# Kernel optimization log

Hardware: AMD Instinct MI355X
Metric: run time of the kernel (lower is better)

The kernel has to match this reference:

```python
import jax, jax.numpy as jnp
import numpy as np

B, N, D, H, K = 8, 1024, 1024, 64, 20


def setup_inputs() -> dict:
    key = jax.random.key(0)
    ks = jax.random.split(key, 8)
    s = 0.05
    return {
        "f1": jax.random.normal(ks[0], (B, N, D), jnp.float32),
        "f2": jax.random.normal(ks[1], (B, N, D), jnp.float32),
        "W1a": jax.random.normal(ks[2], (D, H), jnp.float32) * s,
        "b1a": jnp.zeros((H,), jnp.float32),
        "W2a": jax.random.normal(ks[3], (H, H), jnp.float32) * s,
        "b2a": jnp.zeros((H,), jnp.float32),
        "W1b": jax.random.normal(ks[4], (H, H), jnp.float32) * s,
        "b1b": jnp.zeros((H,), jnp.float32),
        "W2b": jax.random.normal(ks[5], (H, H), jnp.float32) * s,
        "b2b": jnp.zeros((H,), jnp.float32),
        "k": K,
    }


def _knn_idx(f, k):
    # f: [N, D] -> indices [N, k] of k nearest neighbors (self excluded)
    sq = jnp.sum(f * f, axis=-1)                      # [N]
    d = sq[:, None] + sq[None, :] - 2.0 * (f @ f.T)   # [N, N] squared dists
    n = f.shape[0]
    d = d + jnp.eye(n, dtype=f.dtype) * jnp.float32(1e10)  # exclude self-loop
    _, idx = jax.lax.top_k(-d, k)                     # smallest distances
    return idx


def _gin_layer(x, idx, W1, b1, W2, b2):
    # GINConv with eps=0: MLP(x + sum_{j in N(i)} x_j)
    agg = jnp.sum(x[idx], axis=1)                     # [N, D] neighbor-sum
    h = x + agg
    h = jnp.maximum(h @ W1 + b1, 0.0) @ W2 + b2
    return h


def reference(f1, f2, W1a, b1a, W2a, b2a, W1b, b1b, W2b, b2b, k):
    def encode(f):
        idx = _knn_idx(f, k)
        h = _gin_layer(f, idx, W1a, b1a, W2a, b2a)
        h = _gin_layer(h, idx, W1b, b1b, W2b, b2b)
        return h

    def per_sample(a, b):
        z1 = encode(a)                                # [N, H]
        z2 = encode(b)                                # [N, H]
        sim = z1 @ z2.T                               # [N, N]
        return jax.nn.softmax(sim, axis=1)

    return jax.vmap(per_sample)(f1, f2)               # [B, N, N]
```

## Files before the change

### kernel.cpp

```cpp
#include <hip/hip_runtime.h>
#include <hip/hip_bf16.h>
#include <math.h>

#define BATCH 8
#define NPTS  1024
#define DIM   1024
#define HID   64
#define KNN   20
#define NMAT  16
#define KPACK 3072

typedef __attribute__((ext_vector_type(8))) short short8;
typedef __attribute__((ext_vector_type(4))) float floatx4;

__device__ __forceinline__ const float* mat_base(const float* f1, const float* f2, int m) {
    return (m < BATCH) ? (f1 + (size_t)m * NPTS * DIM)
                       : (f2 + (size_t)(m - BATCH) * NPTS * DIM);
}

__device__ __forceinline__ unsigned short f2bf_bits(float v) {
    __hip_bfloat16 h = __float2bfloat16(v);
    return *(unsigned short*)&h;
}
__device__ __forceinline__ float bfbits2f(unsigned short b) {
    union { unsigned u; float f; } c; c.u = ((unsigned)b) << 16; return c.f;
}

__global__ __launch_bounds__(256) void split_ymlp_kernel(const float* __restrict__ f1,
                                                         const float* __restrict__ f2,
                                                         const float* __restrict__ W,
                                                         unsigned short* __restrict__ H,
                                                         float* __restrict__ sq,
                                                         float* __restrict__ y) {
    int row0 = blockIdx.x * 64;
    int m = row0 >> 10;
    const float* A = mat_base(f1, f2, m) + (size_t)(row0 & (NPTS - 1)) * DIM;
    unsigned short* Hb = H + (size_t)row0 * KPACK;
    __shared__ float As[64][20];
    __shared__ float Ws[16][HID];
    int tid = threadIdx.x;
    int r = tid >> 2, cq = (tid & 3) * 4;
    int ty = tid >> 4, tx = tid & 15;
    float acc[4][4];
    #pragma unroll
    for (int i = 0; i < 4; ++i)
        #pragma unroll
        for (int j = 0; j < 4; ++j) acc[i][j] = 0.f;
    float sqp = 0.f;
    unsigned short* Hr = Hb + (size_t)r * KPACK + cq;

    for (int kk = 0; kk < DIM; kk += 16) {
        float4 a = *(const float4*)&A[(size_t)r * DIM + kk + cq];
        {
            float vv[4] = {a.x, a.y, a.z, a.w};
            unsigned short h1[4], h2[4], h3[4];
            #pragma unroll
            for (int c = 0; c < 4; ++c) {
                unsigned short b1 = f2bf_bits(vv[c]);
                float r1 = vv[c] - bfbits2f(b1);
                unsigned short b2 = f2bf_bits(r1);
                float r2 = r1 - bfbits2f(b2);
                unsigned short b3 = f2bf_bits(r2);
                h1[c] = b1; h2[c] = b2; h3[c] = b3;
            }
            *(ushort4*)&Hr[kk]        = *(ushort4*)&h1[0];
            *(ushort4*)&Hr[1024 + kk] = *(ushort4*)&h2[0];
            *(ushort4*)&Hr[2048 + kk] = *(ushort4*)&h3[0];
            sqp += a.x * a.x + a.y * a.y + a.z * a.z + a.w * a.w;
        }
        *(float4*)&As[r][cq] = a;
        {
            int d = tid >> 4, hh = (tid & 15) * 4;
            *(float4*)&Ws[d][hh] = *(const float4*)&W[(size_t)(kk + d) * HID + hh];
        }
        __syncthreads();
        #pragma unroll
        for (int k = 0; k < 16; ++k) {
            float av[4];
            #pragma unroll
            for (int ii = 0; ii < 4; ++ii) av[ii] = As[ty * 4 + ii][k];
            float4 w = *(const float4*)&Ws[k][tx * 4];
            #pragma unroll
            for (int ii = 0; ii < 4; ++ii) {
                acc[ii][0] += av[ii] * w.x;
                acc[ii][1] += av[ii] * w.y;
                acc[ii][2] += av[ii] * w.z;
                acc[ii][3] += av[ii] * w.w;
            }
        }
        __syncthreads();
    }
    sqp += __shfl_down(sqp, 1);
    sqp += __shfl_down(sqp, 2);
    if ((tid & 3) == 0) sq[row0 + r] = sqp;
    #pragma unroll
    for (int ii = 0; ii < 4; ++ii)
        *(float4*)&y[(size_t)(row0 + ty * 4 + ii) * HID + tx * 4] = *(float4*)&acc[ii][0];
}

__global__ __launch_bounds__(256) void gram_mfma_kernel(const unsigned short* __restrict__ H,
                                                        const float* __restrict__ sq,
                                                        float* __restrict__ dist) {
    int bid = blockIdx.x;
    int xcd = bid & 7;
    int g = bid >> 3;
    int m = xcd + 8 * (g & 1);
    int t = g >> 1;
    int bi = 0;
    { int a = t; while (a >= 8 - bi) { a -= 8 - bi; ++bi; } t = a; }
    int bj = bi + t;
    int ti = bi << 7, tj = bj << 7;

    const unsigned short* Hm = H + (size_t)m * NPTS * KPACK;

    __shared__ __align__(16) unsigned short Asl[24 * 512];
    __shared__ __align__(16) unsigned short Bsl[24 * 512];

    int tid = threadIdx.x;
    int w = tid >> 6, lane = tid & 63;
    int wi = w >> 1, wj = w & 1;
    int r16 = lane & 15, kc = lane >> 4;

    floatx4 acc[4][4];
    #pragma unroll
    for (int a = 0; a < 4; ++a)
        #pragma unroll
        for (int b = 0; b < 4; ++b) acc[a][b] = (floatx4)0.f;

    for (int kk = 0; kk < 1024; kk += 32) {
        __syncthreads();
        #pragma unroll
        for (int c = 0; c < 6; ++c) {
            int ca = w * 6 + c;
            int seg = ca >> 3;
            int rb  = ca & 7;
            size_t koff = (size_t)(seg << 10) + kk + kc * 8;
            const unsigned short* ga = Hm + (size_t)(ti + rb * 16 + r16) * KPACK + koff;
            const unsigned short* gb = Hm + (size_t)(tj + rb * 16 + r16) * KPACK + koff;
            __builtin_amdgcn_global_load_lds(
                (const __attribute__((address_space(1))) void*)ga,
                (__attribute__((address_space(3))) void*)&Asl[ca * 512], 16, 0, 0);
            __builtin_amdgcn_global_load_lds(
                (const __attribute__((address_space(1))) void*)gb,
                (__attribute__((address_space(3))) void*)&Bsl[ca * 512], 16, 0, 0);
        }
        __syncthreads();
        short8 af[3][4];
        #pragma unroll
        for (int s = 0; s < 3; ++s)
            #pragma unroll
            for (int a = 0; a < 4; ++a)
                af[s][a] = *(const short8*)&Asl[(s * 8 + wi * 4 + a) * 512 + lane * 8];
        #pragma unroll
        for (int sb = 0; sb < 3; ++sb) {
            short8 bf[4];
            #pragma unroll
            for (int b = 0; b < 4; ++b)
                bf[b] = *(const short8*)&Bsl[(sb * 8 + wj * 4 + b) * 512 + lane * 8];
            #pragma unroll
            for (int sa = 0; sa < 3; ++sa) {
                if (sa + sb > 2) continue;
                #pragma unroll
                for (int a = 0; a < 4; ++a)
                    #pragma unroll
                    for (int b = 0; b < 4; ++b)
                        acc[a][b] = __builtin_amdgcn_mfma_f32_16x16x32_bf16(af[sa][a], bf[b], acc[a][b], 0, 0, 0);
            }
        }
    }

    const float* sqm = sq + m * NPTS;
    #pragma unroll
    for (int a = 0; a < 4; ++a) {
        int i0 = ti + wi * 64 + a * 16 + (lane >> 4) * 4;
        #pragma unroll
        for (int b = 0; b < 4; ++b) {
            int j = tj + wj * 64 + b * 16 + (lane & 15);
            float sqj = sqm[j];
            #pragma unroll
            for (int r = 0; r < 4; ++r) {
                int i = i0 + r;
                float v = sqm[i] + sqj - 2.f * acc[a][b][r];
                if (i == j) v += 1e10f;
                dist[((size_t)m * NPTS + i) * NPTS + j] = v;
                if (bi != bj) dist[((size_t)m * NPTS + j) * NPTS + i] = v;
            }
        }
    }
}

__global__ __launch_bounds__(256) void topk_kernel(const float* __restrict__ dist,
                                                   int* __restrict__ knn_idx) {
    int tid = threadIdx.x;
    int wave = tid >> 6, lane = tid & 63;
    int row = blockIdx.x * 4 + wave;
    const float* d = dist + (size_t)row * NPTS;
    float v[16];
    #pragma unroll
    for (int s = 0; s < 16; ++s) v[s] = d[s * 64 + lane];
    int myj = 0;
    for (int sel = 0; sel < KNN; ++sel) {
        float bv = v[0]; int bs = 0;
        #pragma unroll
        for (int s = 1; s < 16; ++s)
            if (v[s] < bv) { bv = v[s]; bs = s; }
        int bj = bs * 64 + lane;
        #pragma unroll
        for (int off = 1; off < 64; off <<= 1) {
            float ov = __shfl_xor(bv, off);
            int   oj = __shfl_xor(bj, off);
            if (ov < bv || (ov == bv && oj < bj)) { bv = ov; bj = oj; }
        }
        if ((bj & 63) == lane) v[bj >> 6] = 3e38f;
        if (lane == sel) myj = bj;
    }
    if (lane < KNN) knn_idx[(size_t)row * KNN + lane] = myj;
}

__global__ __launch_bounds__(256) void t1h1_kernel(const float* __restrict__ y,
                                                   const int* __restrict__ knn_idx,
                                                   const float* __restrict__ W,
                                                   const float* __restrict__ bias1,
                                                   const float* __restrict__ bias2,
                                                   float* __restrict__ h1) {
    int row0 = blockIdx.x * 64;
    int m = row0 >> 10;
    __shared__ int nb[64 * KNN];
    __shared__ float t1s[64][65];
    __shared__ float Ws[64][HID];
    __shared__ float b1s[HID], b2s[HID];
    int tid = threadIdx.x;
    for (int k = tid; k < 64 * KNN; k += 256) nb[k] = knn_idx[(size_t)row0 * KNN + k];
    for (int k = tid; k < 64 * HID; k += 256) Ws[k >> 6][k & 63] = W[k];
    if (tid < HID) { b1s[tid] = bias1[tid]; b2s[tid] = bias2[tid]; }
    __syncthreads();
    {
        int r = tid >> 2, c0 = (tid & 3) * 16;
        const float* yr = y + (size_t)(row0 + r) * HID + c0;
        float4 a[4];
        #pragma unroll
        for (int q = 0; q < 4; ++q) a[q] = *(const float4*)&yr[q * 4];
        const float* ym = y + (size_t)(m << 10) * HID;
        #pragma unroll
        for (int t = 0; t < KNN; ++t) {
            const float* yn = ym + (size_t)nb[r * KNN + t] * HID + c0;
            #pragma unroll
            for (int q = 0; q < 4; ++q) {
                float4 v = *(const float4*)&yn[q * 4];
                a[q].x += v.x; a[q].y += v.y; a[q].z += v.z; a[q].w += v.w;
            }
        }
        #pragma unroll
        for (int q = 0; q < 4; ++q) {
            int c = c0 + q * 4;
            t1s[r][c + 0] = fmaxf(a[q].x + b1s[c + 0], 0.f);
            t1s[r][c + 1] = fmaxf(a[q].y + b1s[c + 1], 0.f);
            t1s[r][c + 2] = fmaxf(a[q].z + b1s[c + 2], 0.f);
            t1s[r][c + 3] = fmaxf(a[q].w + b1s[c + 3], 0.f);
        }
    }
    __syncthreads();
    int ty = tid >> 4, tx = tid & 15;
    float acc[4][4];
    #pragma unroll
    for (int i = 0; i < 4; ++i)
        #pragma unroll
        for (int j = 0; j < 4; ++j) acc[i][j] = 0.f;
    #pragma unroll
    for (int k = 0; k < HID; ++k) {
        float a[4];
        #pragma unroll
        for (int ii = 0; ii < 4; ++ii) a[ii] = t1s[ty * 4 + ii][k];
        float4 w = *(const float4*)&Ws[k][tx * 4];
        #pragma unroll
        for (int ii = 0; ii < 4; ++ii) {
            acc[ii][0] += a[ii] * w.x;
            acc[ii][1] += a[ii] * w.y;
            acc[ii][2] += a[ii] * w.z;
            acc[ii][3] += a[ii] * w.w;
        }
    }
    #pragma unroll
    for (int ii = 0; ii < 4; ++ii) {
        float o[4];
        #pragma unroll
        for (int jj = 0; jj < 4; ++jj) o[jj] = acc[ii][jj] + b2s[tx * 4 + jj];
        *(float4*)&h1[(size_t)(row0 + ty * 4 + ii) * HID + tx * 4] = *(float4*)&o[0];
    }
}

__global__ __launch_bounds__(256) void t2z_kernel(const float* __restrict__ h1,
                                                  const int* __restrict__ knn_idx,
                                                  const float* __restrict__ W1,
                                                  const float* __restrict__ bias1,
                                                  const float* __restrict__ W2,
                                                  const float* __restrict__ bias2,
                                                  float* __restrict__ z) {
    int row0 = blockIdx.x * 64;
    int m = row0 >> 10;
    __shared__ int nb[64 * KNN];
    __shared__ float hs[64][65];
    __shared__ float t2s[64][65];
    __shared__ float Ws[64][HID];
    __shared__ float b1s[HID], b2s[HID];
    int tid = threadIdx.x;
    for (int k = tid; k < 64 * KNN; k += 256) nb[k] = knn_idx[(size_t)row0 * KNN + k];
    for (int k = tid; k < 64 * HID; k += 256) Ws[k >> 6][k & 63] = W1[k];
    if (tid < HID) { b1s[tid] = bias1[tid]; b2s[tid] = bias2[tid]; }
    __syncthreads();
    {
        int r = tid >> 2, c0 = (tid & 3) * 16;
        const float* hr = h1 + (size_t)(row0 + r) * HID + c0;
        float4 a[4];
        #pragma unroll
        for (int q = 0; q < 4; ++q) a[q] = *(const float4*)&hr[q * 4];
        const float* hm = h1 + (size_t)(m << 10) * HID;
        #pragma unroll
        for (int t = 0; t < KNN; ++t) {
            const float* hn = hm + (size_t)nb[r * KNN + t] * HID + c0;
            #pragma unroll
            for (int q = 0; q < 4; ++q) {
                float4 v = *(const float4*)&hn[q * 4];
                a[q].x += v.x; a[q].y += v.y; a[q].z += v.z; a[q].w += v.w;
            }
        }
        #pragma unroll
        for (int q = 0; q < 4; ++q) *(float4*)&hs[r][c0 + q * 4] = a[q];
    }
    __syncthreads();
    int ty = tid >> 4, tx = tid & 15;
    float acc[4][4];
    #pragma unroll
    for (int i = 0; i < 4; ++i)
        #pragma unroll
        for (int j = 0; j < 4; ++j) acc[i][j] = 0.f;
    #pragma unroll
    for (int k = 0; k < HID; ++k) {
        float a[4];
        #pragma unroll
        for (int ii = 0; ii < 4; ++ii) a[ii] = hs[ty * 4 + ii][k];
        float4 w = *(const float4*)&Ws[k][tx * 4];
        #pragma unroll
        for (int ii = 0; ii < 4; ++ii) {
            acc[ii][0] += a[ii] * w.x;
            acc[ii][1] += a[ii] * w.y;
            acc[ii][2] += a[ii] * w.z;
            acc[ii][3] += a[ii] * w.w;
        }
    }
    #pragma unroll
    for (int ii = 0; ii < 4; ++ii)
        #pragma unroll
        for (int jj = 0; jj < 4; ++jj)
            t2s[ty * 4 + ii][tx * 4 + jj] = fmaxf(acc[ii][jj] + b1s[tx * 4 + jj], 0.f);
    __syncthreads();
    for (int k = tid; k < 64 * HID; k += 256) Ws[k >> 6][k & 63] = W2[k];
    __syncthreads();
    #pragma unroll
    for (int i = 0; i < 4; ++i)
        #pragma unroll
        for (int j = 0; j < 4; ++j) acc[i][j] = 0.f;
    #pragma unroll
    for (int k = 0; k < HID; ++k) {
        float a[4];
        #pragma unroll
        for (int ii = 0; ii < 4; ++ii) a[ii] = t2s[ty * 4 + ii][k];
        float4 w = *(const float4*)&Ws[k][tx * 4];
        #pragma unroll
        for (int ii = 0; ii < 4; ++ii) {
            acc[ii][0] += a[ii] * w.x;
            acc[ii][1] += a[ii] * w.y;
            acc[ii][2] += a[ii] * w.z;
            acc[ii][3] += a[ii] * w.w;
        }
    }
    #pragma unroll
    for (int ii = 0; ii < 4; ++ii) {
        float o[4];
        #pragma unroll
        for (int jj = 0; jj < 4; ++jj) o[jj] = acc[ii][jj] + b2s[tx * 4 + jj];
        *(float4*)&z[(size_t)(row0 + ty * 4 + ii) * HID + tx * 4] = *(float4*)&o[0];
    }
}

__global__ __launch_bounds__(256) void sim_kernel(const float* __restrict__ z,
                                                  float* __restrict__ logits) {
    int bid = blockIdx.x;
    int b = bid >> 8;
    int tile = bid & 255;
    int ti = (tile >> 4) << 6;
    int tj = (tile & 15) << 6;
    const float* z1 = z + (size_t)b * NPTS * HID;
    const float* z2 = z + (size_t)(BATCH + b) * NPTS * HID;
    __shared__ float Z1[64][68];
    __shared__ float Z2[64][68];
    int tid = threadIdx.x;
    #pragma unroll
    for (int i = 0; i < 4; ++i) {
        int l = tid + i * 256;
        int r = l >> 4, c = (l & 15) * 4;
        *(float4*)&Z1[r][c] = *(const float4*)&z1[(size_t)(ti + r) * HID + c];
        *(float4*)&Z2[r][c] = *(const float4*)&z2[(size_t)(tj + r) * HID + c];
    }
    __syncthreads();
    int ty = tid >> 4, tx = tid & 15;
    float acc[4][4];
    #pragma unroll
    for (int i = 0; i < 4; ++i)
        #pragma unroll
        for (int j = 0; j < 4; ++j) acc[i][j] = 0.f;
    #pragma unroll
    for (int h = 0; h < HID; ++h) {
        float a[4], bb[4];
        #pragma unroll
        for (int ii = 0; ii < 4; ++ii) { a[ii] = Z1[ty * 4 + ii][h]; bb[ii] = Z2[tx * 4 + ii][h]; }
        #pragma unroll
        for (int ii = 0; ii < 4; ++ii)
            #pragma unroll
            for (int jj = 0; jj < 4; ++jj)
                acc[ii][jj] += a[ii] * bb[jj];
    }
    #pragma unroll
    for (int ii = 0; ii < 4; ++ii) {
        float* dst = logits + ((size_t)b * NPTS + ti + ty * 4 + ii) * NPTS + tj + tx * 4;
        *(float4*)&dst[0] = *(float4*)&acc[ii][0];
    }
}

__global__ __launch_bounds__(256) void softmax_kernel(const float* __restrict__ logits,
                                                      float* __restrict__ out) {
    int row = blockIdx.x;
    const float* L = logits + (size_t)row * NPTS;
    __shared__ float buf[NPTS];
    __shared__ float red[8];
    int tid = threadIdx.x;
    int wave = tid >> 6, lane = tid & 63;
    float mx = -3e38f;
    #pragma unroll
    for (int s = 0; s < 4; ++s) {
        float v = L[tid + s * 256];
        buf[tid + s * 256] = v;
        mx = fmaxf(mx, v);
    }
    #pragma unroll
    for (int off = 32; off > 0; off >>= 1) mx = fmaxf(mx, __shfl_down(mx, off));
    if (lane == 0) red[wave] = mx;
    __syncthreads();
    mx = fmaxf(fmaxf(red[0], red[1]), fmaxf(red[2], red[3]));
    float sum = 0.f;
    #pragma unroll
    for (int s = 0; s < 4; ++s) {
        float e = expf(buf[tid + s * 256] - mx);
        buf[tid + s * 256] = e;
        sum += e;
    }
    #pragma unroll
    for (int off = 32; off > 0; off >>= 1) sum += __shfl_down(sum, off);
    if (lane == 0) red[4 + wave] = sum;
    __syncthreads();
    float inv = 1.f / (red[4] + red[5] + red[6] + red[7]);
    #pragma unroll
    for (int s = 0; s < 4; ++s)
        out[(size_t)row * NPTS + tid + s * 256] = buf[tid + s * 256] * inv;
}

extern "C" void kernel_launch(void* const* d_in, const int* in_sizes, int n_in,
                              void* d_out, int out_size, void* d_ws, size_t ws_size,
                              hipStream_t stream) {
    const float* f1  = (const float*)d_in[0];
    const float* f2  = (const float*)d_in[1];
    const float* W1a = (const float*)d_in[2];
    const float* b1a = (const float*)d_in[3];
    const float* W2a = (const float*)d_in[4];
    const float* b2a = (const float*)d_in[5];
    const float* W1b = (const float*)d_in[6];
    const float* b1b = (const float*)d_in[7];
    const float* W2b = (const float*)d_in[8];
    const float* b2b = (const float*)d_in[9];
    float* out = (float*)d_out;

    char* ws = (char*)d_ws;
    unsigned short* H = (unsigned short*)ws;
    float* dist = (float*)(ws + (size_t)NMAT * NPTS * KPACK * sizeof(unsigned short));
    float* sq   = dist + (size_t)NMAT * NPTS * NPTS;
    int*   kidx = (int*)(sq + NMAT * NPTS);
    float* ybuf = (float*)(kidx + NMAT * NPTS * KNN);
    float* h1b  = ybuf + (size_t)NMAT * NPTS * HID;
    float* zb   = h1b + (size_t)NMAT * NPTS * HID;

    split_ymlp_kernel<<<NMAT * NPTS / 64, 256, 0, stream>>>(f1, f2, W1a, H, sq, ybuf);
    gram_mfma_kernel<<<NMAT * 36, 256, 0, stream>>>(H, sq, dist);
    topk_kernel<<<NMAT * NPTS / 4, 256, 0, stream>>>(dist, kidx);
    t1h1_kernel<<<NMAT * NPTS / 64, 256, 0, stream>>>(ybuf, kidx, W2a, b1a, b2a, h1b);
    t2z_kernel<<<NMAT * NPTS / 64, 256, 0, stream>>>(h1b, kidx, W1b, b1b, W2b, b2b, zb);
    sim_kernel<<<BATCH * 256, 256, 0, stream>>>(zb, dist);
    softmax_kernel<<<BATCH * NPTS, 256, 0, stream>>>(dist, out);
}
```

Measured before the change: 539.4 us.

## Split Gram split-K across two block groups with atomic accumulation; fold distance into topk

```diff
diff --git a/kernel.cpp b/kernel.cpp
--- a/kernel.cpp
+++ b/kernel.cpp
@@ -32,26 +32,26 @@
                                                          unsigned short* __restrict__ H,
                                                          float* __restrict__ sq,
                                                          float* __restrict__ y) {
-    int row0 = blockIdx.x * 64;
+    int row0 = blockIdx.x * 32;
     int m = row0 >> 10;
     const float* A = mat_base(f1, f2, m) + (size_t)(row0 & (NPTS - 1)) * DIM;
-    unsigned short* Hb = H + (size_t)row0 * KPACK;
-    __shared__ float As[64][20];
+    __shared__ float As[32][20];
     __shared__ float Ws[16][HID];
     int tid = threadIdx.x;
-    int r = tid >> 2, cq = (tid & 3) * 4;
+    bool ld = tid < 128;
+    int r = (tid & 127) >> 2, cq = (tid & 3) * 4;
     int ty = tid >> 4, tx = tid & 15;
-    float acc[4][4];
-    #pragma unroll
-    for (int i = 0; i < 4; ++i)
+    float acc[2][4];
+    #pragma unroll
+    for (int i = 0; i < 2; ++i)
         #pragma unroll
         for (int j = 0; j < 4; ++j) acc[i][j] = 0.f;
     float sqp = 0.f;
-    unsigned short* Hr = Hb + (size_t)r * KPACK + cq;
+    unsigned short* Hr = H + (size_t)(row0 + r) * KPACK + cq;
 
     for (int kk = 0; kk < DIM; kk += 16) {
-        float4 a = *(const float4*)&A[(size_t)r * DIM + kk + cq];
-        {
+        if (ld) {
+            float4 a = *(const float4*)&A[(size_t)r * DIM + kk + cq];
             float vv[4] = {a.x, a.y, a.z, a.w};
             unsigned short h1[4], h2[4], h3[4];
             #pragma unroll
@@ -67,8 +67,8 @@
             *(ushort4*)&Hr[1024 + kk] = *(ushort4*)&h2[0];
             *(ushort4*)&Hr[2048 + kk] = *(ushort4*)&h3[0];
             sqp += a.x * a.x + a.y * a.y + a.z * a.z + a.w * a.w;
-        }
-        *(float4*)&As[r][cq] = a;
+            *(float4*)&As[r][cq] = a;
+        }
         {
             int d = tid >> 4, hh = (tid & 15) * 4;
             *(float4*)&Ws[d][hh] = *(const float4*)&W[(size_t)(kk + d) * HID + hh];
@@ -76,12 +76,12 @@
         __syncthreads();
         #pragma unroll
         for (int k = 0; k < 16; ++k) {
-            float av[4];
-            #pragma unroll
-            for (int ii = 0; ii < 4; ++ii) av[ii] = As[ty * 4 + ii][k];
+            float av[2];
+            #pragma unroll
+            for (int ii = 0; ii < 2; ++ii) av[ii] = As[ty * 2 + ii][k];
             float4 w = *(const float4*)&Ws[k][tx * 4];
             #pragma unroll
-            for (int ii = 0; ii < 4; ++ii) {
+            for (int ii = 0; ii < 2; ++ii) {
                 acc[ii][0] += av[ii] * w.x;
                 acc[ii][1] += av[ii] * w.y;
                 acc[ii][2] += av[ii] * w.z;
@@ -90,22 +90,25 @@
         }
         __syncthreads();
     }
-    sqp += __shfl_down(sqp, 1);
-    sqp += __shfl_down(sqp, 2);
-    if ((tid & 3) == 0) sq[row0 + r] = sqp;
-    #pragma unroll
-    for (int ii = 0; ii < 4; ++ii)
-        *(float4*)&y[(size_t)(row0 + ty * 4 + ii) * HID + tx * 4] = *(float4*)&acc[ii][0];
+    if (ld) {
+        sqp += __shfl_down(sqp, 1);
+        sqp += __shfl_down(sqp, 2);
+        if ((tid & 3) == 0) sq[row0 + r] = sqp;
+    }
+    #pragma unroll
+    for (int ii = 0; ii < 2; ++ii)
+        *(float4*)&y[(size_t)(row0 + ty * 2 + ii) * HID + tx * 4] = *(float4*)&acc[ii][0];
 }
 
 __global__ __launch_bounds__(256) void gram_mfma_kernel(const unsigned short* __restrict__ H,
-                                                        const float* __restrict__ sq,
-                                                        float* __restrict__ dist) {
+                                                        float* __restrict__ G) {
     int bid = blockIdx.x;
     int xcd = bid & 7;
     int g = bid >> 3;
     int m = xcd + 8 * (g & 1);
-    int t = g >> 1;
+    int tg = g >> 1;
+    int grp = tg & 1;
+    int t = tg >> 1;
     int bi = 0;
     { int a = t; while (a >= 8 - bi) { a -= 8 - bi; ++bi; } t = a; }
     int bj = bi + t;
@@ -113,8 +116,7 @@
 
     const unsigned short* Hm = H + (size_t)m * NPTS * KPACK;
 
-    __shared__ __align__(16) unsigned short Asl[24 * 512];
-    __shared__ __align__(16) unsigned short Bsl[24 * 512];
+    __shared__ __align__(16) unsigned short S[32 * 512];
 
     int tid = threadIdx.x;
     int w = tid >> 6, lane = tid & 63;
@@ -130,74 +132,107 @@
     for (int kk = 0; kk < 1024; kk += 32) {
         __syncthreads();
         #pragma unroll
-        for (int c = 0; c < 6; ++c) {
-            int ca = w * 6 + c;
-            int seg = ca >> 3;
-            int rb  = ca & 7;
-            size_t koff = (size_t)(seg << 10) + kk + kc * 8;
-            const unsigned short* ga = Hm + (size_t)(ti + rb * 16 + r16) * KPACK + koff;
-            const unsigned short* gb = Hm + (size_t)(tj + rb * 16 + r16) * KPACK + koff;
+        for (int c = 0; c < 8; ++c) {
+            int ca = w * 8 + c;
+            int isB, seg, rb = ca & 7;
+            if (grp == 0) {
+                isB = ca >= 24;
+                seg = isB ? 0 : (ca >> 3);
+            } else {
+                isB = ca >= 16;
+                seg = isB ? (1 + ((ca >> 3) & 1)) : (ca >> 3);
+            }
+            size_t koff = ((size_t)seg << 10) + kk + kc * 8;
+            int baseRow = (isB ? tj : ti) + rb * 16 + r16;
+            const unsigned short* gp = Hm + (size_t)baseRow * KPACK + koff;
             __builtin_amdgcn_global_load_lds(
-                (const __attribute__((address_space(1))) void*)ga,
-                (__attribute__((address_space(3))) void*)&Asl[ca * 512], 16, 0, 0);
-            __builtin_amdgcn_global_load_lds(
-                (const __attribute__((address_space(1))) void*)gb,
-                (__attribute__((address_space(3))) void*)&Bsl[ca * 512], 16, 0, 0);
+                (const __attribute__((address_space(1))) void*)gp,
+                (__attribute__((address_space(3))) void*)&S[ca * 512], 16, 0, 0);
         }
         __syncthreads();
-        short8 af[3][4];
-        #pragma unroll
-        for (int s = 0; s < 3; ++s)
-            #pragma unroll
-            for (int a = 0; a < 4; ++a)
-                af[s][a] = *(const short8*)&Asl[(s * 8 + wi * 4 + a) * 512 + lane * 8];
-        #pragma unroll
-        for (int sb = 0; sb < 3; ++sb) {
-            short8 bf[4];
+        if (grp == 0) {
+            short8 af[3][4], bf[4];
+            #pragma unroll
+            for (int s = 0; s < 3; ++s)
+                #pragma unroll
+                for (int a = 0; a < 4; ++a)
+                    af[s][a] = *(const short8*)&S[(s * 8 + wi * 4 + a) * 512 + lane * 8];
             #pragma unroll
             for (int b = 0; b < 4; ++b)
-                bf[b] = *(const short8*)&Bsl[(sb * 8 + wj * 4 + b) * 512 + lane * 8];
-            #pragma unroll
-            for (int sa = 0; sa < 3; ++sa) {
-                if (sa + sb > 2) continue;
+                bf[b] = *(const short8*)&S[(24 + wj * 4 + b) * 512 + lane * 8];
+            #pragma unroll
+            for (int sa = 0; sa < 3; ++sa)
                 #pragma unroll
                 for (int a = 0; a < 4; ++a)
                     #pragma unroll
                     for (int b = 0; b < 4; ++b)
                         acc[a][b] = __builtin_amdgcn_mfma_f32_16x16x32_bf16(af[sa][a], bf[b], acc[a][b], 0, 0, 0);
-            }
-        }
-    }
-
-    const float* sqm = sq + m * NPTS;
+        } else {
+            short8 af[2][4], bf1[4], bf2[4];
+            #pragma unroll
+            for (int s = 0; s < 2; ++s)
+                #pragma unroll
+                for (int a = 0; a < 4; ++a)
+                    af[s][a] = *(const short8*)&S[(s * 8 + wi * 4 + a) * 512 + lane * 8];
+            #pragma unroll
+            for (int b = 0; b < 4; ++b) {
+                bf1[b] = *(const short8*)&S[(16 + wj * 4 + b) * 512 + lane * 8];
+                bf2[b] = *(const short8*)&S[(24 + wj * 4 + b) * 512 + lane * 8];
+            }
+            #pragma unroll
+            for (int a = 0; a < 4; ++a)
+                #pragma unroll
+                for (int b = 0; b < 4; ++b)
+                    acc[a][b] = __builtin_amdgcn_mfma_f32_16x16x32_bf16(af[0][a], bf1[b], acc[a][b], 0, 0, 0);
+            #pragma unroll
+            for (int a = 0; a < 4; ++a)
+                #pragma unroll
+                for (int b = 0; b < 4; ++b)
+                    acc[a][b] = __builtin_amdgcn_mfma_f32_16x16x32_bf16(af[1][a], bf1[b], acc[a][b], 0, 0, 0);
+            #pragma unroll
+            for (int a = 0; a < 4; ++a)
+                #pragma unroll
+                for (int b = 0; b < 4; ++b)
+                    acc[a][b] = __builtin_amdgcn_mfma_f32_16x16x32_bf16(af[0][a], bf2[b], acc[a][b], 0, 0, 0);
+        }
+    }
+
+    float* Gm = G + (size_t)m * NPTS * NPTS;
     #pragma unroll
     for (int a = 0; a < 4; ++a) {
         int i0 = ti + wi * 64 + a * 16 + (lane >> 4) * 4;
         #pragma unroll
         for (int b = 0; b < 4; ++b) {
             int j = tj + wj * 64 + b * 16 + (lane & 15);
-            float sqj = sqm[j];
             #pragma unroll
             for (int r = 0; r < 4; ++r) {
                 int i = i0 + r;
-                float v = sqm[i] + sqj - 2.f * acc[a][b][r];
-                if (i == j) v += 1e10f;
-                dist[((size_t)m * NPTS + i) * NPTS + j] = v;
-                if (bi != bj) dist[((size_t)m * NPTS + j) * NPTS + i] = v;
-            }
-        }
-    }
-}
-
-__global__ __launch_bounds__(256) void topk_kernel(const float* __restrict__ dist,
+                float val = acc[a][b][r];
+                atomicAdd(&Gm[(size_t)i * NPTS + j], val);
+                if (bi != bj) atomicAdd(&Gm[(size_t)j * NPTS + i], val);
+            }
+        }
+    }
+}
+
+__global__ __launch_bounds__(256) void topk_kernel(const float* __restrict__ G,
+                                                   const float* __restrict__ sq,
                                                    int* __restrict__ knn_idx) {
     int tid = threadIdx.x;
     int wave = tid >> 6, lane = tid & 63;
     int row = blockIdx.x * 4 + wave;
-    const float* d = dist + (size_t)row * NPTS;
+    int m = row >> 10, iloc = row & (NPTS - 1);
+    const float* g = G + (size_t)row * NPTS;
+    const float* sqm = sq + (m << 10);
+    float sqi = sqm[iloc];
     float v[16];
     #pragma unroll
-    for (int s = 0; s < 16; ++s) v[s] = d[s * 64 + lane];
+    for (int s = 0; s < 16; ++s) {
+        int j = s * 64 + lane;
+        float d = sqi + sqm[j] - 2.f * g[j];
+        if (j == iloc) d += 1e10f;
+        v[s] = d;
+    }
     int myj = 0;
     for (int sel = 0; sel < KNN; ++sel) {
         float bv = v[0]; int bs = 0;
@@ -481,18 +516,19 @@
 
     char* ws = (char*)d_ws;
     unsigned short* H = (unsigned short*)ws;
-    float* dist = (float*)(ws + (size_t)NMAT * NPTS * KPACK * sizeof(unsigned short));
-    float* sq   = dist + (size_t)NMAT * NPTS * NPTS;
+    float* G    = (float*)(ws + (size_t)NMAT * NPTS * KPACK * sizeof(unsigned short));
+    float* sq   = G + (size_t)NMAT * NPTS * NPTS;
     int*   kidx = (int*)(sq + NMAT * NPTS);
     float* ybuf = (float*)(kidx + NMAT * NPTS * KNN);
     float* h1b  = ybuf + (size_t)NMAT * NPTS * HID;
     float* zb   = h1b + (size_t)NMAT * NPTS * HID;
 
-    split_ymlp_kernel<<<NMAT * NPTS / 64, 256, 0, stream>>>(f1, f2, W1a, H, sq, ybuf);
-    gram_mfma_kernel<<<NMAT * 36, 256, 0, stream>>>(H, sq, dist);
-    topk_kernel<<<NMAT * NPTS / 4, 256, 0, stream>>>(dist, kidx);
+    hipMemsetAsync(G, 0, (size_t)NMAT * NPTS * NPTS * sizeof(float), stream);
+    split_ymlp_kernel<<<NMAT * NPTS / 32, 256, 0, stream>>>(f1, f2, W1a, H, sq, ybuf);
+    gram_mfma_kernel<<<NMAT * 36 * 2, 256, 0, stream>>>(H, G);
+    topk_kernel<<<NMAT * NPTS / 4, 256, 0, stream>>>(G, sq, kidx);
     t1h1_kernel<<<NMAT * NPTS / 64, 256, 0, stream>>>(ybuf, kidx, W2a, b1a, b2a, h1b);
     t2z_kernel<<<NMAT * NPTS / 64, 256, 0, stream>>>(h1b, kidx, W1b, b1b, W2b, b2b, zb);
-    sim_kernel<<<BATCH * 256, 256, 0, stream>>>(zb, dist);
-    softmax_kernel<<<BATCH * NPTS, 256, 0, stream>>>(dist, out);
-}
+    sim_kernel<<<BATCH * 256, 256, 0, stream>>>(zb, G);
+    softmax_kernel<<<BATCH * NPTS, 256, 0, stream>>>(G, out);
+}
```

Measured after the change: 716.1 us. 32.8% more time.
